# Optimization experiments

Hardware: AMD Instinct MI355X
Metric: run time of the kernel (lower is better)

Reference implementation:

```python
import jax, jax.numpy as jnp
import numpy as np

BS, OBS_LEN, TS, GW, GH = 1024, 8, 64, 32, 32
HID = 64          # hidden size of both LSTMs (hardcoded in __init__)
TEOM_IN = 36      # 6*6 flattened teom features (zeros in the original forward)


def setup_inputs() -> dict:
    key = jax.random.key(0)
    ks = jax.random.split(key, 22)
    r = lambda k, s, sc=0.1: jax.random.normal(k, s, dtype=jnp.float32) * sc
    return dict(
        obsv=r(ks[0], (BS, OBS_LEN, 2), 1.0),
        teom=jax.random.uniform(ks[1], (BS, TS, GW, GH), dtype=jnp.float32),
        # lstm_obsv (input 2 -> hidden 64), PyTorch gate order i,f,g,o
        Wih_o=r(ks[2], (4 * HID, 2)), Whh_o=r(ks[3], (4 * HID, HID)),
        bih_o=r(ks[4], (4 * HID,)), bhh_o=r(ks[5], (4 * HID,)),
        # lstm_teom (input 36 -> hidden 64)
        Wih_t=r(ks[6], (4 * HID, TEOM_IN)), Whh_t=r(ks[7], (4 * HID, HID)),
        bih_t=r(ks[8], (4 * HID,)), bhh_t=r(ks[9], (4 * HID,)),
        Wof=r(ks[10], (64, HID)), bof=r(ks[11], (64,)),
        Wtf=r(ks[12], (64, HID)), btf=r(ks[13], (64,)),
        Wmix=r(ks[14], (64, 128)), bmix=r(ks[15], (64,)),
        W1=r(ks[16], (32, 64)), b1=r(ks[17], (32,)),
        W2=r(ks[18], (32, 32)), b2=r(ks[19], (32,)),
        W3=r(ks[20], (2, 32)), b3=r(ks[21], (2,)),
    )


def _cell(x, h, c, Wih, Whh, b):
    # standard torch LSTMCell math; b = b_ih + b_hh
    g = x @ Wih.T + h @ Whh.T + b
    i, f, gg, o = jnp.split(g, 4, axis=-1)
    c_new = jax.nn.sigmoid(f) * c + jax.nn.sigmoid(i) * jnp.tanh(gg)
    h_new = jax.nn.sigmoid(o) * jnp.tanh(c_new)
    return h_new, c_new


def reference(obsv, teom, Wih_o, Whh_o, bih_o, bhh_o, Wih_t, Whh_t, bih_t, bhh_t,
              Wof, bof, Wtf, btf, Wmix, bmix, W1, b1, W2, b2, W3, b3):
    bs, out_len = teom.shape[0], teom.shape[1]
    dt = obsv.dtype
    b_o = bih_o + bhh_o
    b_t = bih_t + bhh_t
    # conved_teom_flat is hard zeros in the original forward (convs never called)
    z_teom = jnp.zeros((bs, Wih_t.shape[1]), dt)
    lrelu = lambda v: jnp.where(v >= 0, v, 0.1 * v)  # LeakyReLU(0.1)

    def mix_out(h_t, h_o, buf):
        # buf: [bs, 3, 2] = last three positions (obsv[:,-3:,:])
        ts_ = h_t @ Wtf.T + btf
        os_ = h_o @ Wof.T + bof
        m = jnp.concatenate([ts_, os_], axis=1) @ Wmix.T + bmix
        a = lrelu(m @ W1.T + b1)
        a = lrelu(a @ W2.T + b2)
        o = a @ W3.T + b3
        # y = out(y_mix) + obsv[:,-1,:] + (obsv[:,-1,:] - obsv[:,-3,:]) / 2
        return o + buf[:, -1] + (buf[:, -1] - buf[:, 0]) * 0.5

    h_o = jnp.zeros((bs, HID), dt); c_o = jnp.zeros((bs, HID), dt)
    h_t = jnp.zeros((bs, HID), dt); c_t = jnp.zeros((bs, HID), dt)

    # ---- t == 0: obsv LSTM consumes the full observed trajectory
    def obsv_scan(carry, x_t):
        h, c = carry
        h, c = _cell(x_t, h, c, Wih_o, Whh_o, b_o)
        return (h, c), None
    (h_o, c_o), _ = jax.lax.scan(obsv_scan, (h_o, c_o), obsv.transpose(1, 0, 2))
    h_t, c_t = _cell(z_teom, h_t, c_t, Wih_t, Whh_t, b_t)
    buf = obsv[:, -3:, :]
    y0 = mix_out(h_t, h_o, buf)
    buf = jnp.concatenate([buf[:, 1:], y0[:, None]], axis=1)

    # ---- t = 1 .. out_len-1: obsv LSTM steps on previous prediction
    def step(carry, _):
        h_o, c_o, h_t, c_t, buf = carry
        h_t, c_t = _cell(z_teom, h_t, c_t, Wih_t, Whh_t, b_t)
        h_o, c_o = _cell(buf[:, -1], h_o, c_o, Wih_o, Whh_o, b_o)
        y_t = mix_out(h_t, h_o, buf)
        buf = jnp.concatenate([buf[:, 1:], y_t[:, None]], axis=1)
        return (h_o, c_o, h_t, c_t, buf), y_t

    _, ys = jax.lax.scan(step, (h_o, c_o, h_t, c_t, buf), None, length=out_len - 1)
    y = jnp.concatenate([y0[:, None], ys.transpose(1, 0, 2)], axis=1)  # [bs, out_len, 2]
    # teom_cropped is all-zeros in the original forward -> c is exactly zeros
    c_out = jnp.zeros((bs, out_len), dt)
    return y, c_out
```

## Files before the change

### kernel.cpp

```cpp
#include <hip/hip_runtime.h>

#define BS 1024
#define TS 64

__device__ __forceinline__ float sigf(float x){ return 1.f/(1.f+__expf(-x)); }
__device__ __forceinline__ float tanh_fast(float x){
  float cx = fminf(fmaxf(x,-15.f),15.f);
  float e = __expf(2.f*cx);
  return (e-1.f)/(e+1.f);
}
__device__ __forceinline__ float lrelu(float v){ return v>=0.f ? v : 0.1f*v; }
__device__ __forceinline__ float dot4(float4 a, float4 b){
  return a.x*b.x + a.y*b.y + a.z*b.z + a.w*b.w;
}

__global__ __launch_bounds__(256) void precompute_kernel(
    const float* __restrict__ Whh_t, const float* __restrict__ bih_t,
    const float* __restrict__ bhh_t,
    const float* __restrict__ Wof,  const float* __restrict__ bof,
    const float* __restrict__ Wtf,  const float* __restrict__ btf,
    const float* __restrict__ Wmix, const float* __restrict__ bmix,
    float* __restrict__ ws_wcomb, float* __restrict__ ws_mbias)
{
  __shared__ __align__(16) float sHall[TS*64];
  __shared__ __align__(16) float sTs[TS*64];
  __shared__ float sWof[64*64];
  __shared__ float sG[256];
  __shared__ float sBof[64];
  __shared__ float sCmr[64];

  const int t = threadIdx.x;

  float4 wrow[16];
#pragma unroll
  for (int j=0;j<16;++j) wrow[j] = reinterpret_cast<const float4*>(Whh_t + t*64)[j];
  const float btr = bih_t[t] + bhh_t[t];

  for (int i=t;i<4096;i+=256) sWof[i] = Wof[i];
  if (t<64) sBof[t] = bof[t];
  __syncthreads();

  float c_reg = 0.f;
  for (int s=0;s<TS;++s){
    float a0=btr, a1=0.f, a2=0.f, a3=0.f;
    if (s>0){
      const float4* h4 = reinterpret_cast<const float4*>(sHall + (s-1)*64);
#pragma unroll
      for (int j=0;j<16;j+=4){
        a0 += dot4(wrow[j],   h4[j]);
        a1 += dot4(wrow[j+1], h4[j+1]);
        a2 += dot4(wrow[j+2], h4[j+2]);
        a3 += dot4(wrow[j+3], h4[j+3]);
      }
    }
    sG[t] = (a0+a1)+(a2+a3);
    __syncthreads();
    if (t<64){
      float gi=sG[t], gf=sG[64+t], gg=sG[128+t], go=sG[192+t];
      c_reg = sigf(gf)*c_reg + sigf(gi)*tanh_fast(gg);
      sHall[s*64+t] = sigf(go)*tanh_fast(c_reg);
    }
    __syncthreads();
  }

  if (t<64){
    float acc = bmix[t];
    for (int k=0;k<64;++k) acc += Wmix[t*128+64+k]*sBof[k];
    sCmr[t] = acc;
  }
  for (int o=t;o<TS*64;o+=256){
    int s=o>>6, i=o&63;
    float acc = btf[i];
    for (int k=0;k<64;++k) acc += Wtf[i*64+k]*sHall[s*64+k];
    sTs[o] = acc;
  }
  for (int o=t;o<4096;o+=256){
    int r=o>>6, j=o&63;
    float acc = 0.f;
    for (int k=0;k<64;++k) acc += Wmix[r*128+64+k]*sWof[k*64+j];
    ws_wcomb[o] = acc;
  }
  __syncthreads();
  for (int o=t;o<TS*64;o+=256){
    int s=o>>6, j=o&63;
    float acc = sCmr[j];
    for (int k=0;k<64;++k) acc += Wmix[j*128+k]*sTs[s*64+k];
    ws_mbias[o] = acc;
  }
}

__global__ __launch_bounds__(256, 2) void main_kernel(
    const float* __restrict__ obsv,
    const float* __restrict__ Wih_o, const float* __restrict__ Whh_o,
    const float* __restrict__ bih_o, const float* __restrict__ bhh_o,
    const float* __restrict__ W1, const float* __restrict__ b1,
    const float* __restrict__ W2, const float* __restrict__ b2,
    const float* __restrict__ W3, const float* __restrict__ b3,
    const float* __restrict__ wcomb, const float* __restrict__ mbias,
    float* __restrict__ out)
{
  __shared__ __align__(16) float4 sWc[16*64];
  __shared__ __align__(16) float4 sW1[16*32];
  __shared__ __align__(16) float4 sW2[8*32];
  __shared__ float sG[2*256];
  __shared__ __align__(16) float sH[2*64];
  __shared__ __align__(16) float sM[2*64];
  __shared__ __align__(16) float sA1[2*32];
  __shared__ float sY[2*2];
  __shared__ float sObs[2*16];

  const int t    = threadIdx.x;
  const int blk  = blockIdx.x;
  const int lane = t & 63;
  const int w    = t >> 6;
  const bool tailw = (w < 2);

  if (t < 128) out[BS*TS*2 + blk*128 + t] = 0.f;

  float4 wrow[16];
#pragma unroll
  for (int j=0;j<16;++j) wrow[j] = reinterpret_cast<const float4*>(Whh_o + t*64)[j];
  const float wi0  = Wih_o[2*t];
  const float wi1  = Wih_o[2*t+1];
  const float b_or = bih_o[t] + bhh_o[t];

  for (int i=t;i<1024;i+=256) sWc[i] = reinterpret_cast<const float4*>(wcomb)[(i&63)*16 + (i>>6)];
  for (int i=t;i<512;i+=256)  sW1[i] = reinterpret_cast<const float4*>(W1)[(i&31)*16 + (i>>5)];
  if (t<256)                  sW2[t] = reinterpret_cast<const float4*>(W2)[(t&31)*8 + (t>>5)];
  if (t<32)  sObs[t] = obsv[blk*32 + t];
  if (t<128) sH[t] = 0.f;
  __syncthreads();

  const int rr = lane & 31, hf = lane >> 5;
  const float b1r = b1[rr], b2r = b2[rr];
  const float w30 = W3[rr], w31 = W3[32+rr];
  const float b30 = b3[0],  b31 = b3[1];
  float bl00=0,bl01=0,bl10=0,bl11=0,bl20=0,bl21=0;
  if (tailw){
    bl00 = sObs[w*16+10]; bl01 = sObs[w*16+11];
    bl10 = sObs[w*16+12]; bl11 = sObs[w*16+13];
    bl20 = sObs[w*16+14]; bl21 = sObs[w*16+15];
  }
  float c_reg = 0.f;

  const float4* sH4  = reinterpret_cast<const float4*>(sH);
  const float4* sM4  = reinterpret_cast<const float4*>(sM);
  const float4* sA14 = reinterpret_cast<const float4*>(sA1);

  for (int it=0; it<71; ++it){
    float mb = 0.f;
    if (tailw && it >= 7) mb = mbias[(it-7)*64 + lane];

    float x00,x01,x10,x11;
    if (it < 8){
      x00 = sObs[2*it];    x01 = sObs[2*it+1];
      x10 = sObs[16+2*it]; x11 = sObs[16+2*it+1];
    } else {
      x00 = sY[0]; x01 = sY[1]; x10 = sY[2]; x11 = sY[3];
    }
    float a0 = b_or + wi0*x00 + wi1*x01, p0 = 0.f;
    float a1 = b_or + wi0*x10 + wi1*x11, p1 = 0.f;
#pragma unroll
    for (int q=0;q<16;q+=2){
      const float4 wa = wrow[q], wb = wrow[q+1];
      a0 += dot4(wa, sH4[q]);      p0 += dot4(wb, sH4[q+1]);
      a1 += dot4(wa, sH4[16+q]);   p1 += dot4(wb, sH4[16+q+1]);
    }
    sG[t]     = a0 + p0;
    sG[256+t] = a1 + p1;
    __syncthreads();

    if (tailw){
      __builtin_amdgcn_s_setprio(1);
      const float g0 = sG[w*256+lane],     g1 = sG[w*256+64+lane];
      const float g2 = sG[w*256+128+lane], g3 = sG[w*256+192+lane];
      c_reg = sigf(g1)*c_reg + sigf(g0)*tanh_fast(g2);
      const float h = sigf(g3)*tanh_fast(c_reg);
      sH[w*64+lane] = h;
      __builtin_amdgcn_wave_barrier();

      if (it >= 7){
        const float4* sHw4 = reinterpret_cast<const float4*>(sH + w*64);
        float m0 = mb, m1 = 0.f, m2 = 0.f, m3 = 0.f;
#pragma unroll
        for (int q=0;q<16;q+=4){
          m0 += dot4(sWc[q*64+lane],     sHw4[q]);
          m1 += dot4(sWc[(q+1)*64+lane], sHw4[q+1]);
          m2 += dot4(sWc[(q+2)*64+lane], sHw4[q+2]);
          m3 += dot4(sWc[(q+3)*64+lane], sHw4[q+3]);
        }
        sM[w*64+lane] = (m0+m1)+(m2+m3);
        __builtin_amdgcn_wave_barrier();

        float u = 0.f;
#pragma unroll
        for (int q=0;q<8;++q) u += dot4(sW1[(hf*8+q)*32+rr], sM4[w*16 + hf*8 + q]);
        u += __shfl_xor(u, 32);
        if (lane < 32) sA1[w*32+lane] = lrelu(u + b1r);
        __builtin_amdgcn_wave_barrier();

        float v = 0.f;
#pragma unroll
        for (int q=0;q<4;++q) v += dot4(sW2[(hf*4+q)*32+rr], sA14[w*8 + hf*4 + q]);
        v += __shfl_xor(v, 32);
        const float a2v = lrelu(v + b2r);

        float q0 = a2v*w30, q1 = a2v*w31;
#pragma unroll
        for (int m=1;m<=16;m<<=1){
          q0 += __shfl_xor(q0, m);
          q1 += __shfl_xor(q1, m);
        }
        const float y0 = q0 + b30 + bl20 + (bl20 - bl00)*0.5f;
        const float y1 = q1 + b31 + bl21 + (bl21 - bl01)*0.5f;
        bl00 = bl10; bl01 = bl11;
        bl10 = bl20; bl11 = bl21;
        bl20 = y0;   bl21 = y1;
        if (lane == 0){
          sY[w*2+0] = y0; sY[w*2+1] = y1;
          *reinterpret_cast<float2*>(out + (size_t)((blk*2+w)*TS + (it-7))*2)
              = make_float2(y0, y1);
        }
      }
      __builtin_amdgcn_s_setprio(0);
    }
    __syncthreads();
  }
}

extern "C" void kernel_launch(void* const* d_in, const int* in_sizes, int n_in,
                              void* d_out, int out_size, void* d_ws, size_t ws_size,
                              hipStream_t stream)
{
  const float* obsv  = (const float*)d_in[0];
  const float* Wih_o = (const float*)d_in[2];
  const float* Whh_o = (const float*)d_in[3];
  const float* bih_o = (const float*)d_in[4];
  const float* bhh_o = (const float*)d_in[5];
  const float* Whh_t = (const float*)d_in[7];
  const float* bih_t = (const float*)d_in[8];
  const float* bhh_t = (const float*)d_in[9];
  const float* Wof   = (const float*)d_in[10];
  const float* bof   = (const float*)d_in[11];
  const float* Wtf   = (const float*)d_in[12];
  const float* btf   = (const float*)d_in[13];
  const float* Wmix  = (const float*)d_in[14];
  const float* bmix  = (const float*)d_in[15];
  const float* W1    = (const float*)d_in[16];
  const float* b1    = (const float*)d_in[17];
  const float* W2    = (const float*)d_in[18];
  const float* b2    = (const float*)d_in[19];
  const float* W3    = (const float*)d_in[20];
  const float* b3    = (const float*)d_in[21];

  float* wsf = (float*)d_ws;

  precompute_kernel<<<1,256,0,stream>>>(Whh_t,bih_t,bhh_t,Wof,bof,Wtf,btf,
                                        Wmix,bmix, wsf, wsf+4096);
  main_kernel<<<BS/2,256,0,stream>>>(obsv,Wih_o,Whh_o,bih_o,bhh_o,
                                     W1,b1,W2,b2,W3,b3,
                                     wsf, wsf+4096,
                                     (float*)d_out);
}
```

Before: 577.8 us.

## Give each wave all four gate rows to drop block-wide barriers

Result: slower. 601.2 us (+4.0%).

```diff
diff --git a/kernel.cpp b/kernel.cpp
--- a/kernel.cpp
+++ b/kernel.cpp
@@ -89,7 +89,7 @@
   }
 }
 
-__global__ __launch_bounds__(256, 2) void main_kernel(
+__global__ __launch_bounds__(128, 1) void main_kernel(
     const float* __restrict__ obsv,
     const float* __restrict__ Wih_o, const float* __restrict__ Whh_o,
     const float* __restrict__ bih_o, const float* __restrict__ bhh_o,
@@ -102,129 +102,126 @@
   __shared__ __align__(16) float4 sWc[16*64];
   __shared__ __align__(16) float4 sW1[16*32];
   __shared__ __align__(16) float4 sW2[8*32];
-  __shared__ float sG[2*256];
-  __shared__ __align__(16) float sH[2*64];
+  __shared__ __align__(16) float sHb[2*64];
   __shared__ __align__(16) float sM[2*64];
   __shared__ __align__(16) float sA1[2*32];
-  __shared__ float sY[2*2];
   __shared__ float sObs[2*16];
 
   const int t    = threadIdx.x;
   const int blk  = blockIdx.x;
   const int lane = t & 63;
   const int w    = t >> 6;
-  const bool tailw = (w < 2);
-
-  if (t < 128) out[BS*TS*2 + blk*128 + t] = 0.f;
-
-  float4 wrow[16];
-#pragma unroll
-  for (int j=0;j<16;++j) wrow[j] = reinterpret_cast<const float4*>(Whh_o + t*64)[j];
-  const float wi0  = Wih_o[2*t];
-  const float wi1  = Wih_o[2*t+1];
-  const float b_or = bih_o[t] + bhh_o[t];
-
-  for (int i=t;i<1024;i+=256) sWc[i] = reinterpret_cast<const float4*>(wcomb)[(i&63)*16 + (i>>6)];
-  for (int i=t;i<512;i+=256)  sW1[i] = reinterpret_cast<const float4*>(W1)[(i&31)*16 + (i>>5)];
-  if (t<256)                  sW2[t] = reinterpret_cast<const float4*>(W2)[(t&31)*8 + (t>>5)];
-  if (t<32)  sObs[t] = obsv[blk*32 + t];
-  if (t<128) sH[t] = 0.f;
-  __syncthreads();
+
+  out[BS*TS*2 + blk*128 + t] = 0.f;
+
+  for (int i=t;i<1024;i+=128) sWc[i] = reinterpret_cast<const float4*>(wcomb)[(i&63)*16 + (i>>6)];
+  for (int i=t;i<512;i+=128)  sW1[i] = reinterpret_cast<const float4*>(W1)[(i&31)*16 + (i>>5)];
+  for (int i=t;i<256;i+=128)  sW2[i] = reinterpret_cast<const float4*>(W2)[(i&31)*8 + (i>>5)];
+  if (t<32) sObs[t] = obsv[blk*32 + t];
+  sHb[t] = 0.f;
+
+  const int rI = lane, rF = 64+lane, rG = 128+lane, rO = 192+lane;
+  float4 wI[16], wF[16], wG[16], wO[16];
+#pragma unroll
+  for (int j=0;j<16;++j){
+    wI[j] = reinterpret_cast<const float4*>(Whh_o + rI*64)[j];
+    wF[j] = reinterpret_cast<const float4*>(Whh_o + rF*64)[j];
+    wG[j] = reinterpret_cast<const float4*>(Whh_o + rG*64)[j];
+    wO[j] = reinterpret_cast<const float4*>(Whh_o + rO*64)[j];
+  }
+  const float wiI0=Wih_o[2*rI], wiI1=Wih_o[2*rI+1];
+  const float wiF0=Wih_o[2*rF], wiF1=Wih_o[2*rF+1];
+  const float wiG0=Wih_o[2*rG], wiG1=Wih_o[2*rG+1];
+  const float wiO0=Wih_o[2*rO], wiO1=Wih_o[2*rO+1];
+  const float bI=bih_o[rI]+bhh_o[rI];
+  const float bF=bih_o[rF]+bhh_o[rF];
+  const float bG=bih_o[rG]+bhh_o[rG];
+  const float bO=bih_o[rO]+bhh_o[rO];
 
   const int rr = lane & 31, hf = lane >> 5;
   const float b1r = b1[rr], b2r = b2[rr];
   const float w30 = W3[rr], w31 = W3[32+rr];
   const float b30 = b3[0],  b31 = b3[1];
-  float bl00=0,bl01=0,bl10=0,bl11=0,bl20=0,bl21=0;
-  if (tailw){
-    bl00 = sObs[w*16+10]; bl01 = sObs[w*16+11];
-    bl10 = sObs[w*16+12]; bl11 = sObs[w*16+13];
-    bl20 = sObs[w*16+14]; bl21 = sObs[w*16+15];
-  }
-  float c_reg = 0.f;
-
-  const float4* sH4  = reinterpret_cast<const float4*>(sH);
-  const float4* sM4  = reinterpret_cast<const float4*>(sM);
-  const float4* sA14 = reinterpret_cast<const float4*>(sA1);
+
+  __syncthreads();
+
+  float bl00 = sObs[w*16+10], bl01 = sObs[w*16+11];
+  float bl10 = sObs[w*16+12], bl11 = sObs[w*16+13];
+  float bl20 = sObs[w*16+14], bl21 = sObs[w*16+15];
+  float c_reg = 0.f, y0r = 0.f, y1r = 0.f;
+
+  const float4* sH4w  = reinterpret_cast<const float4*>(sHb + w*64);
+  const float4* sM4w  = reinterpret_cast<const float4*>(sM  + w*64);
+  const float4* sA14w = reinterpret_cast<const float4*>(sA1 + w*32);
 
   for (int it=0; it<71; ++it){
     float mb = 0.f;
-    if (tailw && it >= 7) mb = mbias[(it-7)*64 + lane];
-
-    float x00,x01,x10,x11;
-    if (it < 8){
-      x00 = sObs[2*it];    x01 = sObs[2*it+1];
-      x10 = sObs[16+2*it]; x11 = sObs[16+2*it+1];
-    } else {
-      x00 = sY[0]; x01 = sY[1]; x10 = sY[2]; x11 = sY[3];
-    }
-    float a0 = b_or + wi0*x00 + wi1*x01, p0 = 0.f;
-    float a1 = b_or + wi0*x10 + wi1*x11, p1 = 0.f;
+    if (it >= 7) mb = mbias[(it-7)*64 + lane];
+
+    float x0, x1;
+    if (it < 8){ x0 = sObs[w*16+2*it]; x1 = sObs[w*16+2*it+1]; }
+    else       { x0 = y0r;             x1 = y1r; }
+
+    float aI = bI + wiI0*x0 + wiI1*x1, pI = 0.f;
+    float aF = bF + wiF0*x0 + wiF1*x1, pF = 0.f;
+    float aG = bG + wiG0*x0 + wiG1*x1, pG = 0.f;
+    float aO = bO + wiO0*x0 + wiO1*x1, pO = 0.f;
 #pragma unroll
     for (int q=0;q<16;q+=2){
-      const float4 wa = wrow[q], wb = wrow[q+1];
-      a0 += dot4(wa, sH4[q]);      p0 += dot4(wb, sH4[q+1]);
-      a1 += dot4(wa, sH4[16+q]);   p1 += dot4(wb, sH4[16+q+1]);
-    }
-    sG[t]     = a0 + p0;
-    sG[256+t] = a1 + p1;
-    __syncthreads();
-
-    if (tailw){
-      __builtin_amdgcn_s_setprio(1);
-      const float g0 = sG[w*256+lane],     g1 = sG[w*256+64+lane];
-      const float g2 = sG[w*256+128+lane], g3 = sG[w*256+192+lane];
-      c_reg = sigf(g1)*c_reg + sigf(g0)*tanh_fast(g2);
-      const float h = sigf(g3)*tanh_fast(c_reg);
-      sH[w*64+lane] = h;
+      const float4 h0 = sH4w[q], h1 = sH4w[q+1];
+      aI += dot4(wI[q],h0);  pI += dot4(wI[q+1],h1);
+      aF += dot4(wF[q],h0);  pF += dot4(wF[q+1],h1);
+      aG += dot4(wG[q],h0);  pG += dot4(wG[q+1],h1);
+      aO += dot4(wO[q],h0);  pO += dot4(wO[q+1],h1);
+    }
+    const float gI = aI+pI, gF = aF+pF, gG = aG+pG, gO = aO+pO;
+
+    c_reg = sigf(gF)*c_reg + sigf(gI)*tanh_fast(gG);
+    const float h = sigf(gO)*tanh_fast(c_reg);
+    sHb[w*64+lane] = h;
+    __builtin_amdgcn_wave_barrier();
+
+    if (it >= 7){
+      float m0 = mb, m1 = 0.f, m2 = 0.f, m3 = 0.f;
+#pragma unroll
+      for (int q=0;q<16;q+=4){
+        m0 += dot4(sWc[q*64+lane],     sH4w[q]);
+        m1 += dot4(sWc[(q+1)*64+lane], sH4w[q+1]);
+        m2 += dot4(sWc[(q+2)*64+lane], sH4w[q+2]);
+        m3 += dot4(sWc[(q+3)*64+lane], sH4w[q+3]);
+      }
+      sM[w*64+lane] = (m0+m1)+(m2+m3);
       __builtin_amdgcn_wave_barrier();
 
-      if (it >= 7){
-        const float4* sHw4 = reinterpret_cast<const float4*>(sH + w*64);
-        float m0 = mb, m1 = 0.f, m2 = 0.f, m3 = 0.f;
-#pragma unroll
-        for (int q=0;q<16;q+=4){
-          m0 += dot4(sWc[q*64+lane],     sHw4[q]);
-          m1 += dot4(sWc[(q+1)*64+lane], sHw4[q+1]);
-          m2 += dot4(sWc[(q+2)*64+lane], sHw4[q+2]);
-          m3 += dot4(sWc[(q+3)*64+lane], sHw4[q+3]);
-        }
-        sM[w*64+lane] = (m0+m1)+(m2+m3);
-        __builtin_amdgcn_wave_barrier();
-
-        float u = 0.f;
-#pragma unroll
-        for (int q=0;q<8;++q) u += dot4(sW1[(hf*8+q)*32+rr], sM4[w*16 + hf*8 + q]);
-        u += __shfl_xor(u, 32);
-        if (lane < 32) sA1[w*32+lane] = lrelu(u + b1r);
-        __builtin_amdgcn_wave_barrier();
-
-        float v = 0.f;
-#pragma unroll
-        for (int q=0;q<4;++q) v += dot4(sW2[(hf*4+q)*32+rr], sA14[w*8 + hf*4 + q]);
-        v += __shfl_xor(v, 32);
-        const float a2v = lrelu(v + b2r);
-
-        float q0 = a2v*w30, q1 = a2v*w31;
-#pragma unroll
-        for (int m=1;m<=16;m<<=1){
-          q0 += __shfl_xor(q0, m);
-          q1 += __shfl_xor(q1, m);
-        }
-        const float y0 = q0 + b30 + bl20 + (bl20 - bl00)*0.5f;
-        const float y1 = q1 + b31 + bl21 + (bl21 - bl01)*0.5f;
-        bl00 = bl10; bl01 = bl11;
-        bl10 = bl20; bl11 = bl21;
-        bl20 = y0;   bl21 = y1;
-        if (lane == 0){
-          sY[w*2+0] = y0; sY[w*2+1] = y1;
-          *reinterpret_cast<float2*>(out + (size_t)((blk*2+w)*TS + (it-7))*2)
-              = make_float2(y0, y1);
-        }
+      float u = 0.f;
+#pragma unroll
+      for (int q=0;q<8;++q) u += dot4(sW1[(hf*8+q)*32+rr], sM4w[hf*8+q]);
+      u += __shfl_xor(u, 32);
+      if (lane < 32) sA1[w*32+lane] = lrelu(u + b1r);
+      __builtin_amdgcn_wave_barrier();
+
+      float v = 0.f;
+#pragma unroll
+      for (int q=0;q<4;++q) v += dot4(sW2[(hf*4+q)*32+rr], sA14w[hf*4+q]);
+      v += __shfl_xor(v, 32);
+      const float a2v = lrelu(v + b2r);
+
+      float q0 = a2v*w30, q1 = a2v*w31;
+#pragma unroll
+      for (int m=1;m<=16;m<<=1){
+        q0 += __shfl_xor(q0, m);
+        q1 += __shfl_xor(q1, m);
       }
-      __builtin_amdgcn_s_setprio(0);
-    }
-    __syncthreads();
+      const float y0 = q0 + b30 + bl20 + (bl20 - bl00)*0.5f;
+      const float y1 = q1 + b31 + bl21 + (bl21 - bl01)*0.5f;
+      bl00 = bl10; bl01 = bl11;
+      bl10 = bl20; bl11 = bl21;
+      bl20 = y0;   bl21 = y1;
+      y0r = y0;    y1r = y1;
+      if (lane == 0)
+        *reinterpret_cast<float2*>(out + (size_t)((blk*2+w)*TS + (it-7))*2)
+            = make_float2(y0, y1);
+    }
   }
 }
 
@@ -257,7 +254,7 @@
 
   precompute_kernel<<<1,256,0,stream>>>(Whh_t,bih_t,bhh_t,Wof,bof,Wtf,btf,
                                         Wmix,bmix, wsf, wsf+4096);
-  main_kernel<<<BS/2,256,0,stream>>>(obsv,Wih_o,Whh_o,bih_o,bhh_o,
+  main_kernel<<<BS/2,128,0,stream>>>(obsv,Wih_o,Whh_o,bih_o,bhh_o,
                                      W1,b1,W2,b2,W3,b3,
                                      wsf, wsf+4096,
                                      (float*)d_out);
```

## Process four batch rows per block so all waves run the tail

Applied to the files above, without the earlier changes.

After: 682.1 us. +18.1%, slower.

```diff
diff --git a/kernel.cpp b/kernel.cpp
--- a/kernel.cpp
+++ b/kernel.cpp
@@ -89,7 +89,7 @@
   }
 }
 
-__global__ __launch_bounds__(256, 2) void main_kernel(
+__global__ __launch_bounds__(256, 1) void main_kernel(
     const float* __restrict__ obsv,
     const float* __restrict__ Wih_o, const float* __restrict__ Whh_o,
     const float* __restrict__ bih_o, const float* __restrict__ bhh_o,
@@ -102,20 +102,25 @@
   __shared__ __align__(16) float4 sWc[16*64];
   __shared__ __align__(16) float4 sW1[16*32];
   __shared__ __align__(16) float4 sW2[8*32];
-  __shared__ float sG[2*256];
-  __shared__ __align__(16) float sH[2*64];
-  __shared__ __align__(16) float sM[2*64];
-  __shared__ __align__(16) float sA1[2*32];
-  __shared__ float sY[2*2];
-  __shared__ float sObs[2*16];
+  __shared__ float sG[4*256];
+  __shared__ __align__(16) float sHb[4*64];
+  __shared__ __align__(16) float sM[4*64];
+  __shared__ __align__(16) float sA1[4*32];
+  __shared__ float sY[4*2];
+  __shared__ float sObs[4*16];
 
   const int t    = threadIdx.x;
   const int blk  = blockIdx.x;
   const int lane = t & 63;
   const int w    = t >> 6;
-  const bool tailw = (w < 2);
-
-  if (t < 128) out[BS*TS*2 + blk*128 + t] = 0.f;
+
+  out[BS*TS*2 + blk*256 + t] = 0.f;
+
+  for (int i=t;i<1024;i+=256) sWc[i] = reinterpret_cast<const float4*>(wcomb)[(i&63)*16 + (i>>6)];
+  for (int i=t;i<512;i+=256)  sW1[i] = reinterpret_cast<const float4*>(W1)[(i&31)*16 + (i>>5)];
+  if (t<256)                  sW2[t] = reinterpret_cast<const float4*>(W2)[(t&31)*8 + (t>>5)];
+  if (t<64) sObs[t] = obsv[blk*64 + t];
+  sHb[t] = 0.f;
 
   float4 wrow[16];
 #pragma unroll
@@ -124,84 +129,88 @@
   const float wi1  = Wih_o[2*t+1];
   const float b_or = bih_o[t] + bhh_o[t];
 
-  for (int i=t;i<1024;i+=256) sWc[i] = reinterpret_cast<const float4*>(wcomb)[(i&63)*16 + (i>>6)];
-  for (int i=t;i<512;i+=256)  sW1[i] = reinterpret_cast<const float4*>(W1)[(i&31)*16 + (i>>5)];
-  if (t<256)                  sW2[t] = reinterpret_cast<const float4*>(W2)[(t&31)*8 + (t>>5)];
-  if (t<32)  sObs[t] = obsv[blk*32 + t];
-  if (t<128) sH[t] = 0.f;
-  __syncthreads();
-
   const int rr = lane & 31, hf = lane >> 5;
   const float b1r = b1[rr], b2r = b2[rr];
   const float w30 = W3[rr], w31 = W3[32+rr];
   const float b30 = b3[0],  b31 = b3[1];
-  float bl00=0,bl01=0,bl10=0,bl11=0,bl20=0,bl21=0;
-  if (tailw){
-    bl00 = sObs[w*16+10]; bl01 = sObs[w*16+11];
-    bl10 = sObs[w*16+12]; bl11 = sObs[w*16+13];
-    bl20 = sObs[w*16+14]; bl21 = sObs[w*16+15];
-  }
+
+  __syncthreads();
+
+  float bl00 = sObs[w*16+10], bl01 = sObs[w*16+11];
+  float bl10 = sObs[w*16+12], bl11 = sObs[w*16+13];
+  float bl20 = sObs[w*16+14], bl21 = sObs[w*16+15];
   float c_reg = 0.f;
 
-  const float4* sH4  = reinterpret_cast<const float4*>(sH);
-  const float4* sM4  = reinterpret_cast<const float4*>(sM);
-  const float4* sA14 = reinterpret_cast<const float4*>(sA1);
+  const float4* sH4   = reinterpret_cast<const float4*>(sHb);
+  const float4* sH4w  = reinterpret_cast<const float4*>(sHb + w*64);
+  const float4* sM4w  = reinterpret_cast<const float4*>(sM  + w*64);
+  const float4* sA14w = reinterpret_cast<const float4*>(sA1 + w*32);
 
   for (int it=0; it<71; ++it){
     float mb = 0.f;
-    if (tailw && it >= 7) mb = mbias[(it-7)*64 + lane];
-
-    float x00,x01,x10,x11;
-    if (it < 8){
-      x00 = sObs[2*it];    x01 = sObs[2*it+1];
-      x10 = sObs[16+2*it]; x11 = sObs[16+2*it+1];
-    } else {
-      x00 = sY[0]; x01 = sY[1]; x10 = sY[2]; x11 = sY[3];
-    }
-    float a0 = b_or + wi0*x00 + wi1*x01, p0 = 0.f;
-    float a1 = b_or + wi0*x10 + wi1*x11, p1 = 0.f;
+    if (it >= 7) mb = mbias[(it-7)*64 + lane];
+
+    float a0,a1,a2,a3,p0,p1,p2,p3;
+    {
+      float x00,x01,x10,x11,x20,x21,x30,x31;
+      if (it < 8){
+        x00=sObs[   2*it]; x01=sObs[   2*it+1];
+        x10=sObs[16+2*it]; x11=sObs[16+2*it+1];
+        x20=sObs[32+2*it]; x21=sObs[32+2*it+1];
+        x30=sObs[48+2*it]; x31=sObs[48+2*it+1];
+      } else {
+        x00=sY[0]; x01=sY[1]; x10=sY[2]; x11=sY[3];
+        x20=sY[4]; x21=sY[5]; x30=sY[6]; x31=sY[7];
+      }
+      a0 = b_or + wi0*x00 + wi1*x01; p0 = 0.f;
+      a1 = b_or + wi0*x10 + wi1*x11; p1 = 0.f;
+      a2 = b_or + wi0*x20 + wi1*x21; p2 = 0.f;
+      a3 = b_or + wi0*x30 + wi1*x31; p3 = 0.f;
+    }
 #pragma unroll
     for (int q=0;q<16;q+=2){
       const float4 wa = wrow[q], wb = wrow[q+1];
-      a0 += dot4(wa, sH4[q]);      p0 += dot4(wb, sH4[q+1]);
-      a1 += dot4(wa, sH4[16+q]);   p1 += dot4(wb, sH4[16+q+1]);
-    }
-    sG[t]     = a0 + p0;
-    sG[256+t] = a1 + p1;
-    __syncthreads();
-
-    if (tailw){
-      __builtin_amdgcn_s_setprio(1);
+      a0 += dot4(wa, sH4[q]);       p0 += dot4(wb, sH4[q+1]);
+      a1 += dot4(wa, sH4[16+q]);    p1 += dot4(wb, sH4[16+q+1]);
+      a2 += dot4(wa, sH4[32+q]);    p2 += dot4(wb, sH4[32+q+1]);
+      a3 += dot4(wa, sH4[48+q]);    p3 += dot4(wb, sH4[48+q+1]);
+    }
+    sG[      t] = a0 + p0;
+    sG[256 + t] = a1 + p1;
+    sG[512 + t] = a2 + p2;
+    sG[768 + t] = a3 + p3;
+    __syncthreads();
+
+    {
       const float g0 = sG[w*256+lane],     g1 = sG[w*256+64+lane];
       const float g2 = sG[w*256+128+lane], g3 = sG[w*256+192+lane];
       c_reg = sigf(g1)*c_reg + sigf(g0)*tanh_fast(g2);
       const float h = sigf(g3)*tanh_fast(c_reg);
-      sH[w*64+lane] = h;
+      sHb[w*64+lane] = h;
       __builtin_amdgcn_wave_barrier();
 
       if (it >= 7){
-        const float4* sHw4 = reinterpret_cast<const float4*>(sH + w*64);
         float m0 = mb, m1 = 0.f, m2 = 0.f, m3 = 0.f;
 #pragma unroll
         for (int q=0;q<16;q+=4){
-          m0 += dot4(sWc[q*64+lane],     sHw4[q]);
-          m1 += dot4(sWc[(q+1)*64+lane], sHw4[q+1]);
-          m2 += dot4(sWc[(q+2)*64+lane], sHw4[q+2]);
-          m3 += dot4(sWc[(q+3)*64+lane], sHw4[q+3]);
+          m0 += dot4(sWc[q*64+lane],     sH4w[q]);
+          m1 += dot4(sWc[(q+1)*64+lane], sH4w[q+1]);
+          m2 += dot4(sWc[(q+2)*64+lane], sH4w[q+2]);
+          m3 += dot4(sWc[(q+3)*64+lane], sH4w[q+3]);
         }
         sM[w*64+lane] = (m0+m1)+(m2+m3);
         __builtin_amdgcn_wave_barrier();
 
         float u = 0.f;
 #pragma unroll
-        for (int q=0;q<8;++q) u += dot4(sW1[(hf*8+q)*32+rr], sM4[w*16 + hf*8 + q]);
+        for (int q=0;q<8;++q) u += dot4(sW1[(hf*8+q)*32+rr], sM4w[hf*8+q]);
         u += __shfl_xor(u, 32);
         if (lane < 32) sA1[w*32+lane] = lrelu(u + b1r);
         __builtin_amdgcn_wave_barrier();
 
         float v = 0.f;
 #pragma unroll
-        for (int q=0;q<4;++q) v += dot4(sW2[(hf*4+q)*32+rr], sA14[w*8 + hf*4 + q]);
+        for (int q=0;q<4;++q) v += dot4(sW2[(hf*4+q)*32+rr], sA14w[hf*4+q]);
         v += __shfl_xor(v, 32);
         const float a2v = lrelu(v + b2r);
 
@@ -218,11 +227,10 @@
         bl20 = y0;   bl21 = y1;
         if (lane == 0){
           sY[w*2+0] = y0; sY[w*2+1] = y1;
-          *reinterpret_cast<float2*>(out + (size_t)((blk*2+w)*TS + (it-7))*2)
+          *reinterpret_cast<float2*>(out + (size_t)((blk*4+w)*TS + (it-7))*2)
               = make_float2(y0, y1);
         }
       }
-      __builtin_amdgcn_s_setprio(0);
     }
     __syncthreads();
   }
@@ -257,7 +265,7 @@
 
   precompute_kernel<<<1,256,0,stream>>>(Whh_t,bih_t,bhh_t,Wof,bof,Wtf,btf,
                                         Wmix,bmix, wsf, wsf+4096);
-  main_kernel<<<BS/2,256,0,stream>>>(obsv,Wih_o,Whh_o,bih_o,bhh_o,
+  main_kernel<<<BS/4,256,0,stream>>>(obsv,Wih_o,Whh_o,bih_o,bhh_o,
                                      W1,b1,W2,b2,W3,b3,
                                      wsf, wsf+4096,
                                      (float*)d_out);
```

## Process one sequence per block and rotate the tail wave across SIMDs

Applied to the files above, without the earlier changes.

Result: slower. 614.3 us (+6.3%).

```diff
diff --git a/kernel.cpp b/kernel.cpp
--- a/kernel.cpp
+++ b/kernel.cpp
@@ -89,7 +89,7 @@
   }
 }
 
-__global__ __launch_bounds__(256, 2) void main_kernel(
+__global__ __launch_bounds__(256, 4) void main_kernel(
     const float* __restrict__ obsv,
     const float* __restrict__ Wih_o, const float* __restrict__ Whh_o,
     const float* __restrict__ bih_o, const float* __restrict__ bhh_o,
@@ -102,20 +102,27 @@
   __shared__ __align__(16) float4 sWc[16*64];
   __shared__ __align__(16) float4 sW1[16*32];
   __shared__ __align__(16) float4 sW2[8*32];
-  __shared__ float sG[2*256];
-  __shared__ __align__(16) float sH[2*64];
-  __shared__ __align__(16) float sM[2*64];
-  __shared__ __align__(16) float sA1[2*32];
-  __shared__ float sY[2*2];
-  __shared__ float sObs[2*16];
+  __shared__ float sG[256];
+  __shared__ __align__(16) float sHb[64];
+  __shared__ __align__(16) float sM[64];
+  __shared__ __align__(16) float sA1[32];
+  __shared__ float sY[2];
+  __shared__ float sObs[16];
 
   const int t    = threadIdx.x;
   const int blk  = blockIdx.x;
   const int lane = t & 63;
   const int w    = t >> 6;
-  const bool tailw = (w < 2);
-
-  if (t < 128) out[BS*TS*2 + blk*128 + t] = 0.f;
+  const int tw   = (blk + (blk >> 8)) & 3;
+  const bool tailw = (w == tw);
+
+  if (t < 64) out[BS*TS*2 + blk*64 + t] = 0.f;
+
+  for (int i=t;i<1024;i+=256) sWc[i] = reinterpret_cast<const float4*>(wcomb)[(i&63)*16 + (i>>6)];
+  for (int i=t;i<512;i+=256)  sW1[i] = reinterpret_cast<const float4*>(W1)[(i&31)*16 + (i>>5)];
+  if (t<256)                  sW2[t] = reinterpret_cast<const float4*>(W2)[(t&31)*8 + (t>>5)];
+  if (t<16) sObs[t] = obsv[blk*16 + t];
+  if (t<64) sHb[t] = 0.f;
 
   float4 wrow[16];
 #pragma unroll
@@ -123,85 +130,73 @@
   const float wi0  = Wih_o[2*t];
   const float wi1  = Wih_o[2*t+1];
   const float b_or = bih_o[t] + bhh_o[t];
-
-  for (int i=t;i<1024;i+=256) sWc[i] = reinterpret_cast<const float4*>(wcomb)[(i&63)*16 + (i>>6)];
-  for (int i=t;i<512;i+=256)  sW1[i] = reinterpret_cast<const float4*>(W1)[(i&31)*16 + (i>>5)];
-  if (t<256)                  sW2[t] = reinterpret_cast<const float4*>(W2)[(t&31)*8 + (t>>5)];
-  if (t<32)  sObs[t] = obsv[blk*32 + t];
-  if (t<128) sH[t] = 0.f;
-  __syncthreads();
 
   const int rr = lane & 31, hf = lane >> 5;
   const float b1r = b1[rr], b2r = b2[rr];
   const float w30 = W3[rr], w31 = W3[32+rr];
   const float b30 = b3[0],  b31 = b3[1];
   float bl00=0,bl01=0,bl10=0,bl11=0,bl20=0,bl21=0;
+  float c_reg = 0.f;
+
+  __syncthreads();
+
   if (tailw){
-    bl00 = sObs[w*16+10]; bl01 = sObs[w*16+11];
-    bl10 = sObs[w*16+12]; bl11 = sObs[w*16+13];
-    bl20 = sObs[w*16+14]; bl21 = sObs[w*16+15];
-  }
-  float c_reg = 0.f;
-
-  const float4* sH4  = reinterpret_cast<const float4*>(sH);
-  const float4* sM4  = reinterpret_cast<const float4*>(sM);
-  const float4* sA14 = reinterpret_cast<const float4*>(sA1);
+    bl00 = sObs[10]; bl01 = sObs[11];
+    bl10 = sObs[12]; bl11 = sObs[13];
+    bl20 = sObs[14]; bl21 = sObs[15];
+  }
+
+  const float4* sH4   = reinterpret_cast<const float4*>(sHb);
+  const float4* sM4   = reinterpret_cast<const float4*>(sM);
+  const float4* sA14  = reinterpret_cast<const float4*>(sA1);
 
   for (int it=0; it<71; ++it){
     float mb = 0.f;
     if (tailw && it >= 7) mb = mbias[(it-7)*64 + lane];
 
-    float x00,x01,x10,x11;
-    if (it < 8){
-      x00 = sObs[2*it];    x01 = sObs[2*it+1];
-      x10 = sObs[16+2*it]; x11 = sObs[16+2*it+1];
-    } else {
-      x00 = sY[0]; x01 = sY[1]; x10 = sY[2]; x11 = sY[3];
-    }
-    float a0 = b_or + wi0*x00 + wi1*x01, p0 = 0.f;
-    float a1 = b_or + wi0*x10 + wi1*x11, p1 = 0.f;
+    float x0, x1;
+    if (it < 8){ x0 = sObs[2*it]; x1 = sObs[2*it+1]; }
+    else       { x0 = sY[0];      x1 = sY[1]; }
+    float a0 = b_or + wi0*x0 + wi1*x1, p0 = 0.f;
 #pragma unroll
     for (int q=0;q<16;q+=2){
-      const float4 wa = wrow[q], wb = wrow[q+1];
-      a0 += dot4(wa, sH4[q]);      p0 += dot4(wb, sH4[q+1]);
-      a1 += dot4(wa, sH4[16+q]);   p1 += dot4(wb, sH4[16+q+1]);
-    }
-    sG[t]     = a0 + p0;
-    sG[256+t] = a1 + p1;
+      a0 += dot4(wrow[q],   sH4[q]);
+      p0 += dot4(wrow[q+1], sH4[q+1]);
+    }
+    sG[t] = a0 + p0;
     __syncthreads();
 
     if (tailw){
       __builtin_amdgcn_s_setprio(1);
-      const float g0 = sG[w*256+lane],     g1 = sG[w*256+64+lane];
-      const float g2 = sG[w*256+128+lane], g3 = sG[w*256+192+lane];
+      const float g0 = sG[lane],     g1 = sG[64+lane];
+      const float g2 = sG[128+lane], g3 = sG[192+lane];
       c_reg = sigf(g1)*c_reg + sigf(g0)*tanh_fast(g2);
       const float h = sigf(g3)*tanh_fast(c_reg);
-      sH[w*64+lane] = h;
+      sHb[lane] = h;
       __builtin_amdgcn_wave_barrier();
 
       if (it >= 7){
-        const float4* sHw4 = reinterpret_cast<const float4*>(sH + w*64);
         float m0 = mb, m1 = 0.f, m2 = 0.f, m3 = 0.f;
 #pragma unroll
         for (int q=0;q<16;q+=4){
-          m0 += dot4(sWc[q*64+lane],     sHw4[q]);
-          m1 += dot4(sWc[(q+1)*64+lane], sHw4[q+1]);
-          m2 += dot4(sWc[(q+2)*64+lane], sHw4[q+2]);
-          m3 += dot4(sWc[(q+3)*64+lane], sHw4[q+3]);
+          m0 += dot4(sWc[q*64+lane],     sH4[q]);
+          m1 += dot4(sWc[(q+1)*64+lane], sH4[q+1]);
+          m2 += dot4(sWc[(q+2)*64+lane], sH4[q+2]);
+          m3 += dot4(sWc[(q+3)*64+lane], sH4[q+3]);
         }
-        sM[w*64+lane] = (m0+m1)+(m2+m3);
+        sM[lane] = (m0+m1)+(m2+m3);
         __builtin_amdgcn_wave_barrier();
 
         float u = 0.f;
 #pragma unroll
-        for (int q=0;q<8;++q) u += dot4(sW1[(hf*8+q)*32+rr], sM4[w*16 + hf*8 + q]);
+        for (int q=0;q<8;++q) u += dot4(sW1[(hf*8+q)*32+rr], sM4[hf*8+q]);
         u += __shfl_xor(u, 32);
-        if (lane < 32) sA1[w*32+lane] = lrelu(u + b1r);
+        if (lane < 32) sA1[lane] = lrelu(u + b1r);
         __builtin_amdgcn_wave_barrier();
 
         float v = 0.f;
 #pragma unroll
-        for (int q=0;q<4;++q) v += dot4(sW2[(hf*4+q)*32+rr], sA14[w*8 + hf*4 + q]);
+        for (int q=0;q<4;++q) v += dot4(sW2[(hf*4+q)*32+rr], sA14[hf*4+q]);
         v += __shfl_xor(v, 32);
         const float a2v = lrelu(v + b2r);
 
@@ -217,8 +212,8 @@
         bl10 = bl20; bl11 = bl21;
         bl20 = y0;   bl21 = y1;
         if (lane == 0){
-          sY[w*2+0] = y0; sY[w*2+1] = y1;
-          *reinterpret_cast<float2*>(out + (size_t)((blk*2+w)*TS + (it-7))*2)
+          sY[0] = y0; sY[1] = y1;
+          *reinterpret_cast<float2*>(out + (size_t)(blk*TS + (it-7))*2)
               = make_float2(y0, y1);
         }
       }
@@ -257,8 +252,8 @@
 
   precompute_kernel<<<1,256,0,stream>>>(Whh_t,bih_t,bhh_t,Wof,bof,Wtf,btf,
                                         Wmix,bmix, wsf, wsf+4096);
-  main_kernel<<<BS/2,256,0,stream>>>(obsv,Wih_o,Whh_o,bih_o,bhh_o,
-                                     W1,b1,W2,b2,W3,b3,
-                                     wsf, wsf+4096,
-                                     (float*)d_out);
-}
+  main_kernel<<<BS,256,0,stream>>>(obsv,Wih_o,Whh_o,bih_o,bhh_o,
+                                   W1,b1,W2,b2,W3,b3,
+                                   wsf, wsf+4096,
+                                   (float*)d_out);
+}
```
